# Kernel tuning notes

Hardware: AMD Instinct MI355X
Metric: run time of the kernel (lower is better)

Reference implementation:

```python
import jax, jax.numpy as jnp
import numpy as np

DIM = 512
NUM_HEADS = 8
HEAD_DIM = DIM // NUM_HEADS
MAX_FRAMES = 64
EPS = 1e-5


def setup_inputs() -> dict:
    key = jax.random.key(0)
    ks = jax.random.split(key, 6)
    x = jax.random.normal(ks[0], (4, DIM, 16, 32, 32), dtype=jnp.float32)
    W_qkv = jax.random.normal(ks[1], (3 * DIM, DIM), dtype=jnp.float32) * (DIM ** -0.5)
    W_proj = jax.random.normal(ks[2], (DIM, DIM), dtype=jnp.float32) * (DIM ** -0.5)
    b_proj = jnp.zeros((DIM,), dtype=jnp.float32)
    rel_bias = jax.random.normal(ks[3], (MAX_FRAMES, MAX_FRAMES), dtype=jnp.float32) * 0.02
    ln_g = jnp.ones((DIM,), dtype=jnp.float32)
    ln_b = jnp.zeros((DIM,), dtype=jnp.float32)
    return {"x": x, "W_qkv": W_qkv, "W_proj": W_proj, "b_proj": b_proj,
            "rel_bias": rel_bias, "ln_g": ln_g, "ln_b": ln_b}


def reference(x, W_qkv, W_proj, b_proj, rel_bias, ln_g, ln_b):
    B, C, F, H, W = x.shape
    h = NUM_HEADS
    scale = HEAD_DIM ** -0.5
    # (B,C,F,H,W) -> (B*H*W, F, C)
    xr = jnp.transpose(x, (0, 3, 4, 2, 1)).reshape(B * H * W, F, C)
    residual = xr
    # LayerNorm over channel dim
    mu = jnp.mean(xr, axis=-1, keepdims=True)
    var = jnp.mean(jnp.square(xr - mu), axis=-1, keepdims=True)
    xn = (xr - mu) * jax.lax.rsqrt(var + EPS) * ln_g + ln_b
    # QKV projection (torch Linear: x @ W.T)
    qkv = xn @ W_qkv.T  # (BHW, F, 3C)
    q, k, v = jnp.split(qkv, 3, axis=-1)
    split_heads = lambda t: t.reshape(t.shape[0], F, h, HEAD_DIM).transpose(0, 2, 1, 3)
    q, k, v = split_heads(q), split_heads(k), split_heads(v)  # (BHW, h, F, d)
    attn = jnp.einsum('bhid,bhjd->bhij', q, k) * scale + rel_bias[:F, :F]
    attn = jax.nn.softmax(attn, axis=-1)
    out = jnp.einsum('bhij,bhjd->bhid', attn, v)  # (BHW, h, F, d)
    out = out.transpose(0, 2, 1, 3).reshape(B * H * W, F, C)
    out = out @ W_proj.T + b_proj + residual
    # (B*H*W, F, C) -> (B, C, F, H, W)
    out = out.reshape(B, H, W, F, C).transpose(0, 4, 3, 1, 2)
    return out
```

## Files before the change

kernel.cpp:

```cpp
#include <hip/hip_runtime.h>

typedef unsigned short ushort_t;
typedef __attribute__((ext_vector_type(4))) float f32x4;
typedef __attribute__((ext_vector_type(8))) short s16x8;
typedef __attribute__((ext_vector_type(4))) short s16x4;

#define SB 8388608
#define SC 16384
#define SF 1024

static __device__ __forceinline__ float bf2f(ushort_t u) {
    union { float f; unsigned int i; } x; x.i = ((unsigned int)u) << 16; return x.f;
}
static __device__ __forceinline__ ushort_t f2bf(float f) {
    union { float f; unsigned int i; } x; x.f = f;
    unsigned int u = x.i;
    unsigned int r = (u + 0x7FFFu + ((u >> 16) & 1u)) >> 16;
    return (ushort_t)r;
}

static __device__ __forceinline__ void gload16(const void* g, void* l) {
    __builtin_amdgcn_global_load_lds(
        (const __attribute__((address_space(1))) unsigned int*)g,
        (__attribute__((address_space(3))) unsigned int*)l, 16, 0, 0);
}

__global__ void k_cvt(const float* __restrict__ a, int n1,
                      const float* __restrict__ b, int n2,
                      ushort_t* __restrict__ o1, ushort_t* __restrict__ o2) {
    int i = blockIdx.x * blockDim.x + threadIdx.x;
    if (i < n1) o1[i] = f2bf(a[i]);
    if (i < n2) o2[i] = f2bf(b[i]);
}

__global__ __launch_bounds__(256) void k_ln_transpose(
        const float* __restrict__ x, const float* __restrict__ g,
        const float* __restrict__ bta, ushort_t* __restrict__ xn) {
    __shared__ float tile[32 * 513];
    __shared__ float gg[512];
    __shared__ float bb[512];
    int bid = blockIdx.x;
    int b = bid >> 9;
    int f = (bid >> 5) & 15;
    int h = bid & 31;
    int t = threadIdx.x;
    for (int c = t; c < 512; c += 256) { gg[c] = g[c]; bb[c] = bta[c]; }
    const float* xp = x + (size_t)b * SB + (size_t)f * SF + h * 32;
    int wq4 = (t & 7) * 4;
    int c0 = t >> 3;
    for (int it = 0; it < 16; ++it) {
        int c = c0 + it * 32;
        f32x4 v = *(const f32x4*)(xp + (size_t)c * SC + wq4);
        tile[(wq4 + 0) * 513 + c] = v[0];
        tile[(wq4 + 1) * 513 + c] = v[1];
        tile[(wq4 + 2) * 513 + c] = v[2];
        tile[(wq4 + 3) * 513 + c] = v[3];
    }
    __syncthreads();
    int lane = t & 63;
    int wave = t >> 6;
    for (int wi = 0; wi < 8; ++wi) {
        int ww = wave * 8 + wi;
        float s = 0.f, s2 = 0.f;
        #pragma unroll
        for (int j = 0; j < 8; ++j) {
            float v = tile[ww * 513 + lane + j * 64];
            s += v; s2 += v * v;
        }
        #pragma unroll
        for (int off = 32; off; off >>= 1) { s += __shfl_xor(s, off); s2 += __shfl_xor(s2, off); }
        float mean = s * (1.f / 512.f);
        float var = s2 * (1.f / 512.f) - mean * mean;
        float rstd = rsqrtf(var + 1e-5f);
        size_t row = ((size_t)((b * 32 + h) * 32 + ww)) * 16 + f;
        ushort_t* op = xn + row * 512 + lane * 8;
        union { ushort_t a[8]; s16x8 v; } u;
        #pragma unroll
        for (int j = 0; j < 8; ++j) {
            int c = lane * 8 + j;
            float v = tile[ww * 513 + c];
            u.a[j] = f2bf((v - mean) * rstd * gg[c] + bb[c]);
        }
        *(s16x8*)op = u.v;
    }
}

__global__ __launch_bounds__(512) void k_qkv_attn(
        const ushort_t* __restrict__ xn, const ushort_t* __restrict__ wq,
        const float* __restrict__ rb, ushort_t* __restrict__ att) {
    __shared__ __align__(16) char U[50176];
    ushort_t* qsm = (ushort_t*)(U);
    ushort_t* ksm = (ushort_t*)(U + 16384);
    ushort_t* vT  = (ushort_t*)(U + 32768);

    const int t = threadIdx.x;
    const int lane = t & 63;
    const int wv = t >> 6;
    const int l16 = lane & 15;
    const int lg = lane >> 4;
    const int m0 = blockIdx.x * 128;
    const int wm = wv >> 2;
    const int wn = wv & 3;
    ushort_t* psw = ksm + wv * 1024;
    ushort_t* olw = qsm + wv * 1024;

    auto stageA = [&](int buf, int kb) {
        ushort_t* dst = (ushort_t*)(U + buf * 8192);
        int row = t >> 2, slot = t & 3;
        const ushort_t* src = xn + (size_t)(m0 + row) * 512 + kb * 32 + ((slot ^ ((row >> 2) & 3)) << 3);
        gload16(src, dst + t * 8);
    };
    auto stageB = [&](int buf, int kb, int h) {
        ushort_t* dst = (ushort_t*)(U + 16384 + buf * 12288);
        {
            int row = t >> 2, slot = t & 3;
            int wrow = (row >> 6) * 512 + h * 64 + (row & 63);
            const ushort_t* src = wq + (size_t)wrow * 512 + kb * 32 + ((slot ^ ((row >> 2) & 3)) << 3);
            gload16(src, dst + t * 8);
        }
        if (t < 256) {
            int u = t + 512;
            int row = u >> 2, slot = u & 3;
            int wrow = (row >> 6) * 512 + h * 64 + (row & 63);
            const ushort_t* src = wq + (size_t)wrow * 512 + kb * 32 + ((slot ^ ((row >> 2) & 3)) << 3);
            gload16(src, dst + u * 8);
        }
    };

    for (int h = 0; h < 8; ++h) {
        __syncthreads();
        stageA(0, 0); stageB(0, 0, h);
        __syncthreads();

        f32x4 acc[4][3];
        #pragma unroll
        for (int a1 = 0; a1 < 4; ++a1)
            #pragma unroll
            for (int a2 = 0; a2 < 3; ++a2)
                acc[a1][a2] = (f32x4){0.f, 0.f, 0.f, 0.f};

        for (int kb = 0; kb < 16; ++kb) {
            int cur = kb & 1;
            if (kb < 15) { stageA(cur ^ 1, kb + 1); stageB(cur ^ 1, kb + 1, h); }
            const ushort_t* Ac = (const ushort_t*)(U + cur * 8192);
            const ushort_t* Bc = (const ushort_t*)(U + 16384 + cur * 12288);
            s16x8 af[4], bf[3];
            #pragma unroll
            for (int mf = 0; mf < 4; ++mf) {
                int row = wm * 64 + mf * 16 + l16;
                af[mf] = *(const s16x8*)&Ac[row * 32 + ((lg ^ ((row >> 2) & 3)) << 3)];
            }
            #pragma unroll
            for (int nf = 0; nf < 3; ++nf) {
                int nrow = wn * 48 + nf * 16 + l16;
                bf[nf] = *(const s16x8*)&Bc[nrow * 32 + ((lg ^ ((nrow >> 2) & 3)) << 3)];
            }
            #pragma unroll
            for (int mf = 0; mf < 4; ++mf)
                #pragma unroll
                for (int nf = 0; nf < 3; ++nf)
                    acc[mf][nf] = __builtin_amdgcn_mfma_f32_16x16x32_bf16(af[mf], bf[nf], acc[mf][nf], 0, 0, 0);
            __syncthreads();
        }

        #pragma unroll
        for (int mf = 0; mf < 4; ++mf) {
            int mbase = wm * 64 + mf * 16 + lg * 4;
            #pragma unroll
            for (int nf = 0; nf < 3; ++nf) {
                int nn = wn * 48 + nf * 16 + l16;
                int seg = nn >> 6;
                int d = nn & 63;
                if (seg == 2) {
                    union { s16x4 v; ushort_t a[4]; } pk;
                    #pragma unroll
                    for (int r = 0; r < 4; ++r) pk.a[r] = f2bf(acc[mf][nf][r]);
                    *(s16x4*)&vT[d * 136 + mbase] = pk.v;
                } else {
                    ushort_t* dst = seg ? ksm : qsm;
                    #pragma unroll
                    for (int r = 0; r < 4; ++r) {
                        int m = mbase + r;
                        dst[m * 64 + (d ^ ((m & 7) << 3))] = f2bf(acc[mf][nf][r]);
                    }
                }
            }
        }
        __syncthreads();

        {
            int arow = wv * 16 + l16;
            int sw = (arow & 7) << 4;
            f32x4 sacc = (f32x4){0.f, 0.f, 0.f, 0.f};
            #pragma unroll
            for (int kk = 0; kk < 2; ++kk) {
                int off = kk * 64 + lg * 16;
                s16x8 ka = *(const s16x8*)&ksm[arow * 64 + ((off ^ sw) >> 1)];
                s16x8 qb = *(const s16x8*)&qsm[arow * 64 + ((off ^ sw) >> 1)];
                sacc = __builtin_amdgcn_mfma_f32_16x16x32_bf16(ka, qb, sacc, 0, 0, 0);
            }
            const float* rbp = rb + l16 * 64 + lg * 4;
            float p[4];
            float mx = -1e30f;
            #pragma unroll
            for (int r = 0; r < 4; ++r) {
                p[r] = sacc[r] * 0.125f + rbp[r];
                mx = fmaxf(mx, p[r]);
            }
            mx = fmaxf(mx, __shfl_xor(mx, 16));
            mx = fmaxf(mx, __shfl_xor(mx, 32));
            float sum = 0.f;
            #pragma unroll
            for (int r = 0; r < 4; ++r) { p[r] = __expf(p[r] - mx); sum += p[r]; }
            sum += __shfl_xor(sum, 16);
            sum += __shfl_xor(sum, 32);
            float inv = 1.f / sum;
            {
                union { s16x4 v; ushort_t a[4]; } pk;
                #pragma unroll
                for (int r = 0; r < 4; ++r) pk.a[r] = f2bf(p[r] * inv);
                *(s16x4*)&psw[l16 * 16 + lg * 4] = pk.v;
            }
            asm volatile("s_waitcnt lgkmcnt(0)" ::: "memory");
            s16x8 ap = (s16x8){0, 0, 0, 0, 0, 0, 0, 0};
            if (lg < 2) ap = *(const s16x8*)&psw[l16 * 16 + lg * 8];
            int jj = (lg < 2) ? lg * 8 : 0;
            f32x4 ov[4];
            #pragma unroll
            for (int ff = 0; ff < 4; ++ff) {
                int d = ff * 16 + l16;
                s16x8 bv = *(const s16x8*)&vT[d * 136 + wv * 16 + jj];
                ov[ff] = __builtin_amdgcn_mfma_f32_16x16x32_bf16(ap, bv, (f32x4){0.f, 0.f, 0.f, 0.f}, 0, 0, 0);
            }
            #pragma unroll
            for (int ff = 0; ff < 4; ++ff)
                #pragma unroll
                for (int r = 0; r < 4; ++r)
                    olw[(lg * 4 + r) * 64 + ff * 16 + l16] = f2bf(ov[ff][r]);
            asm volatile("s_waitcnt lgkmcnt(0)" ::: "memory");
            {
                int i2 = lane >> 2;
                int c2 = (lane & 3) * 16;
                s16x8 w0 = *(const s16x8*)&olw[i2 * 64 + c2];
                s16x8 w1 = *(const s16x8*)&olw[i2 * 64 + c2 + 8];
                ushort_t* op = att + (size_t)(m0 + wv * 16 + i2) * 512 + h * 64 + c2;
                *(s16x8*)op = w0;
                *(s16x8*)(op + 8) = w1;
            }
        }
    }
}

__global__ __launch_bounds__(512) void k_proj_out(
        const ushort_t* __restrict__ att, const ushort_t* __restrict__ wp,
        const float* __restrict__ bp, const float* __restrict__ x,
        float* __restrict__ out) {
    __shared__ __align__(16) char U[49152];
    int bid = blockIdx.x;
    int nh = bid & 1;
    int fq = (bid >> 1) & 3;
    int h = (bid >> 3) & 31;
    int b = bid >> 8;
    const int n0 = nh * 256;
    const int t = threadIdx.x;
    const int lane = t & 63;
    const int wv = t >> 6;
    const int l16 = lane & 15;
    const int lg = lane >> 4;
    const int wm = wv >> 2;
    const int wn = wv & 3;
    size_t attbase = ((size_t)(b * 32 + h) * 32) * 16 + fq * 4;

    auto stA = [&](int buf, int ks) {
        int row = t >> 2, slot = t & 3;
        int w = row & 31, fl = row >> 5;
        const ushort_t* src = att + (attbase + (size_t)w * 16 + fl) * 512 + ks * 32 + ((slot ^ ((row >> 2) & 3)) << 3);
        gload16(src, (ushort_t*)(U + buf * 8192) + t * 8);
    };
    auto stB = [&](int buf, int ks) {
        #pragma unroll
        for (int i = 0; i < 2; ++i) {
            int u = t + i * 512;
            int row = u >> 2, slot = u & 3;
            const ushort_t* src = wp + (size_t)(n0 + row) * 512 + ks * 32 + ((slot ^ ((row >> 2) & 3)) << 3);
            gload16(src, (ushort_t*)(U + 16384 + buf * 16384) + u * 8);
        }
    };

    f32x4 acc[4][4];
    #pragma unroll
    for (int m = 0; m < 4; ++m)
        #pragma unroll
        for (int n = 0; n < 4; ++n)
            acc[m][n] = (f32x4){0.f, 0.f, 0.f, 0.f};

    stA(0, 0); stB(0, 0);
    __syncthreads();
    for (int ks = 0; ks < 16; ++ks) {
        int cur = ks & 1;
        if (ks < 15) { stA(cur ^ 1, ks + 1); stB(cur ^ 1, ks + 1); }
        s16x8 af[4], bf[4];
        #pragma unroll
        for (int mf = 0; mf < 4; ++mf) {
            int row = wm * 64 + mf * 16 + l16;
            af[mf] = *(const s16x8*)((ushort_t*)(U + cur * 8192) + row * 32 + ((lg ^ ((row >> 2) & 3)) << 3));
        }
        #pragma unroll
        for (int nf = 0; nf < 4; ++nf) {
            int nrow = wn * 64 + nf * 16 + l16;
            bf[nf] = *(const s16x8*)((ushort_t*)(U + 16384 + cur * 16384) + nrow * 32 + ((lg ^ ((nrow >> 2) & 3)) << 3));
        }
        #pragma unroll
        for (int mf = 0; mf < 4; ++mf)
            #pragma unroll
            for (int nf = 0; nf < 4; ++nf)
                acc[mf][nf] = __builtin_amdgcn_mfma_f32_16x16x32_bf16(bf[nf], af[mf], acc[mf][nf], 0, 0, 0);
        __syncthreads();
    }

    size_t obase = (size_t)b * SB + (size_t)(fq * 4) * SF + h * 32;
    #pragma unroll
    for (int mf = 0; mf < 4; ++mf) {
        int m = wm * 64 + mf * 16 + l16;
        int w = m & 31, fl = m >> 5;
        size_t base_m = obase + (size_t)fl * SF + w;
        #pragma unroll
        for (int nf = 0; nf < 4; ++nf) {
            int col0 = n0 + wn * 64 + nf * 16 + lg * 4;
            #pragma unroll
            for (int r = 0; r < 4; ++r) {
                int col = col0 + r;
                size_t a = base_m + (size_t)col * SC;
                out[a] = acc[mf][nf][r] + bp[col] + x[a];
            }
        }
    }
}

extern "C" void kernel_launch(void* const* d_in, const int* in_sizes, int n_in,
                              void* d_out, int out_size, void* d_ws, size_t ws_size,
                              hipStream_t stream) {
    const float* x     = (const float*)d_in[0];
    const float* wqkv  = (const float*)d_in[1];
    const float* wproj = (const float*)d_in[2];
    const float* bproj = (const float*)d_in[3];
    const float* rb    = (const float*)d_in[4];
    const float* lng   = (const float*)d_in[5];
    const float* lnb   = (const float*)d_in[6];
    float* out = (float*)d_out;
    char* ws = (char*)d_ws;
    ushort_t* xn   = (ushort_t*)(ws);
    ushort_t* att  = (ushort_t*)(ws + 67108864);
    ushort_t* wq16 = (ushort_t*)(ws + 134217728);
    ushort_t* wp16 = (ushort_t*)(ws + 135790592);

    k_cvt<<<3072, 256, 0, stream>>>(wqkv, 1536 * 512, wproj, 512 * 512, wq16, wp16);
    k_ln_transpose<<<2048, 256, 0, stream>>>(x, lng, lnb, xn);
    k_qkv_attn<<<512, 512, 0, stream>>>(xn, wq16, rb, att);
    k_proj_out<<<1024, 512, 0, stream>>>(att, wp16, bproj, x, out);
}
```

Measured before the change: 363.4 us.

## Triple-buffer GEMM staging with explicit vmcnt waits and wider K tiles

The QKV GEMM inside the attention kernel now stages 64-wide K tiles in a three-deep LDS ring. It uses explicit s_waitcnt vmcnt counts and raw s_barrier in place of __syncthreads, so loads run two stages ahead. The projection kernel gets the same three-stage ring at its existing K width. The aim is to hide global-load latency and cut barrier and drain overhead per K step. In exchange, LDS use grows a lot (120KB and 72KB per block), which may limit occupancy, and the hand-tuned vmcnt values must match the number of issued loads exactly.

Result: faster. 320.3 us (-11.9%).

```diff
diff --git a/kernel.cpp b/kernel.cpp
--- a/kernel.cpp
+++ b/kernel.cpp
@@ -23,6 +23,12 @@
     __builtin_amdgcn_global_load_lds(
         (const __attribute__((address_space(1))) unsigned int*)g,
         (__attribute__((address_space(3))) unsigned int*)l, 16, 0, 0);
+}
+
+static __device__ __forceinline__ void wg_barrier() {
+    asm volatile("" ::: "memory");
+    __builtin_amdgcn_s_barrier();
+    asm volatile("" ::: "memory");
 }
 
 __global__ void k_cvt(const float* __restrict__ a, int n1,
@@ -88,7 +94,7 @@
 __global__ __launch_bounds__(512) void k_qkv_attn(
         const ushort_t* __restrict__ xn, const ushort_t* __restrict__ wq,
         const float* __restrict__ rb, ushort_t* __restrict__ att) {
-    __shared__ __align__(16) char U[50176];
+    __shared__ __align__(16) char U[122880];
     ushort_t* qsm = (ushort_t*)(U);
     ushort_t* ksm = (ushort_t*)(U + 16384);
     ushort_t* vT  = (ushort_t*)(U + 32768);
@@ -105,32 +111,31 @@
     ushort_t* olw = qsm + wv * 1024;
 
     auto stageA = [&](int buf, int kb) {
-        ushort_t* dst = (ushort_t*)(U + buf * 8192);
-        int row = t >> 2, slot = t & 3;
-        const ushort_t* src = xn + (size_t)(m0 + row) * 512 + kb * 32 + ((slot ^ ((row >> 2) & 3)) << 3);
-        gload16(src, dst + t * 8);
+        ushort_t* dst = (ushort_t*)(U + buf * 16384);
+        #pragma unroll
+        for (int it = 0; it < 2; ++it) {
+            int f = t + it * 512;
+            int row = f >> 3, slot = f & 7;
+            const ushort_t* src = xn + (size_t)(m0 + row) * 512 + kb * 64 + ((slot ^ (row & 7)) << 3);
+            gload16(src, dst + f * 8);
+        }
     };
     auto stageB = [&](int buf, int kb, int h) {
-        ushort_t* dst = (ushort_t*)(U + 16384 + buf * 12288);
-        {
-            int row = t >> 2, slot = t & 3;
-            int wrow = (row >> 6) * 512 + h * 64 + (row & 63);
-            const ushort_t* src = wq + (size_t)wrow * 512 + kb * 32 + ((slot ^ ((row >> 2) & 3)) << 3);
-            gload16(src, dst + t * 8);
-        }
-        if (t < 256) {
-            int u = t + 512;
-            int row = u >> 2, slot = u & 3;
-            int wrow = (row >> 6) * 512 + h * 64 + (row & 63);
-            const ushort_t* src = wq + (size_t)wrow * 512 + kb * 32 + ((slot ^ ((row >> 2) & 3)) << 3);
-            gload16(src, dst + u * 8);
+        ushort_t* dst = (ushort_t*)(U + 49152 + buf * 24576);
+        #pragma unroll
+        for (int it = 0; it < 3; ++it) {
+            int f = t + it * 512;
+            int brow = f >> 3, slot = f & 7;
+            int wrow = (brow >> 6) * 512 + h * 64 + (brow & 63);
+            const ushort_t* src = wq + (size_t)wrow * 512 + kb * 64 + ((slot ^ (brow & 7)) << 3);
+            gload16(src, dst + f * 8);
         }
     };
 
     for (int h = 0; h < 8; ++h) {
         __syncthreads();
         stageA(0, 0); stageB(0, 0, h);
-        __syncthreads();
+        stageA(1, 1); stageB(1, 1, h);
 
         f32x4 acc[4][3];
         #pragma unroll
@@ -139,28 +144,41 @@
             for (int a2 = 0; a2 < 3; ++a2)
                 acc[a1][a2] = (f32x4){0.f, 0.f, 0.f, 0.f};
 
-        for (int kb = 0; kb < 16; ++kb) {
-            int cur = kb & 1;
-            if (kb < 15) { stageA(cur ^ 1, kb + 1); stageB(cur ^ 1, kb + 1, h); }
-            const ushort_t* Ac = (const ushort_t*)(U + cur * 8192);
-            const ushort_t* Bc = (const ushort_t*)(U + 16384 + cur * 12288);
-            s16x8 af[4], bf[3];
-            #pragma unroll
-            for (int mf = 0; mf < 4; ++mf) {
-                int row = wm * 64 + mf * 16 + l16;
-                af[mf] = *(const s16x8*)&Ac[row * 32 + ((lg ^ ((row >> 2) & 3)) << 3)];
-            }
-            #pragma unroll
-            for (int nf = 0; nf < 3; ++nf) {
-                int nrow = wn * 48 + nf * 16 + l16;
-                bf[nf] = *(const s16x8*)&Bc[nrow * 32 + ((lg ^ ((nrow >> 2) & 3)) << 3)];
-            }
-            #pragma unroll
-            for (int mf = 0; mf < 4; ++mf)
-                #pragma unroll
-                for (int nf = 0; nf < 3; ++nf)
-                    acc[mf][nf] = __builtin_amdgcn_mfma_f32_16x16x32_bf16(af[mf], bf[nf], acc[mf][nf], 0, 0, 0);
-            __syncthreads();
+        for (int kb = 0; kb < 8; ++kb) {
+            int cur = kb % 3;
+            if (kb < 6) {
+                stageA((kb + 2) % 3, kb + 2);
+                stageB((kb + 2) % 3, kb + 2, h);
+                asm volatile("s_waitcnt vmcnt(10)" ::: "memory");
+            } else if (kb == 6) {
+                asm volatile("s_waitcnt vmcnt(5)" ::: "memory");
+            } else {
+                asm volatile("s_waitcnt vmcnt(0)" ::: "memory");
+            }
+            wg_barrier();
+            const ushort_t* Ac = (const ushort_t*)(U + cur * 16384);
+            const ushort_t* Bc = (const ushort_t*)(U + 49152 + cur * 24576);
+            #pragma unroll
+            for (int kk = 0; kk < 2; ++kk) {
+                int koff = kk * 64 + lg * 16;
+                s16x8 af[4], bf[3];
+                #pragma unroll
+                for (int mf = 0; mf < 4; ++mf) {
+                    int row = wm * 64 + mf * 16 + l16;
+                    af[mf] = *(const s16x8*)&Ac[row * 64 + ((koff ^ ((row & 7) << 4)) >> 1)];
+                }
+                #pragma unroll
+                for (int nf = 0; nf < 3; ++nf) {
+                    int nrow = wn * 48 + nf * 16 + l16;
+                    bf[nf] = *(const s16x8*)&Bc[nrow * 64 + ((koff ^ ((nrow & 7) << 4)) >> 1)];
+                }
+                #pragma unroll
+                for (int mf = 0; mf < 4; ++mf)
+                    #pragma unroll
+                    for (int nf = 0; nf < 3; ++nf)
+                        acc[mf][nf] = __builtin_amdgcn_mfma_f32_16x16x32_bf16(af[mf], bf[nf], acc[mf][nf], 0, 0, 0);
+            }
+            wg_barrier();
         }
 
         #pragma unroll
@@ -255,7 +273,7 @@
         const ushort_t* __restrict__ att, const ushort_t* __restrict__ wp,
         const float* __restrict__ bp, const float* __restrict__ x,
         float* __restrict__ out) {
-    __shared__ __align__(16) char U[49152];
+    __shared__ __align__(16) char U[73728];
     int bid = blockIdx.x;
     int nh = bid & 1;
     int fq = (bid >> 1) & 3;
@@ -283,7 +301,7 @@
             int u = t + i * 512;
             int row = u >> 2, slot = u & 3;
             const ushort_t* src = wp + (size_t)(n0 + row) * 512 + ks * 32 + ((slot ^ ((row >> 2) & 3)) << 3);
-            gload16(src, (ushort_t*)(U + 16384 + buf * 16384) + u * 8);
+            gload16(src, (ushort_t*)(U + 24576 + buf * 16384) + u * 8);
         }
     };
 
@@ -295,10 +313,19 @@
             acc[m][n] = (f32x4){0.f, 0.f, 0.f, 0.f};
 
     stA(0, 0); stB(0, 0);
-    __syncthreads();
+    stA(1, 1); stB(1, 1);
     for (int ks = 0; ks < 16; ++ks) {
-        int cur = ks & 1;
-        if (ks < 15) { stA(cur ^ 1, ks + 1); stB(cur ^ 1, ks + 1); }
+        int cur = ks % 3;
+        if (ks < 14) {
+            stA((ks + 2) % 3, ks + 2);
+            stB((ks + 2) % 3, ks + 2);
+            asm volatile("s_waitcnt vmcnt(6)" ::: "memory");
+        } else if (ks == 14) {
+            asm volatile("s_waitcnt vmcnt(3)" ::: "memory");
+        } else {
+            asm volatile("s_waitcnt vmcnt(0)" ::: "memory");
+        }
+        wg_barrier();
         s16x8 af[4], bf[4];
         #pragma unroll
         for (int mf = 0; mf < 4; ++mf) {
@@ -308,14 +335,14 @@
         #pragma unroll
         for (int nf = 0; nf < 4; ++nf) {
             int nrow = wn * 64 + nf * 16 + l16;
-            bf[nf] = *(const s16x8*)((ushort_t*)(U + 16384 + cur * 16384) + nrow * 32 + ((lg ^ ((nrow >> 2) & 3)) << 3));
+            bf[nf] = *(const s16x8*)((ushort_t*)(U + 24576 + cur * 16384) + nrow * 32 + ((lg ^ ((nrow >> 2) & 3)) << 3));
         }
         #pragma unroll
         for (int mf = 0; mf < 4; ++mf)
             #pragma unroll
             for (int nf = 0; nf < 4; ++nf)
                 acc[mf][nf] = __builtin_amdgcn_mfma_f32_16x16x32_bf16(bf[nf], af[mf], acc[mf][nf], 0, 0, 0);
-        __syncthreads();
+        wg_barrier();
     }
 
     size_t obase = (size_t)b * SB + (size_t)(fq * 4) * SF + h * 32;
```
